# Kernel optimization log

Hardware: AMD Instinct MI355X
Metric: run time of the kernel (lower is better)

The kernel has to match this reference:

```python
import jax, jax.numpy as jnp
import numpy as np

N = 16383        # complete binary tree, 14 levels
D_NODE = 512
D_SSM = 512
D_STATE = 16
MAX_DEPTH = 14   # number of BFS levels (depth 0..13)
LN_EPS = 1e-5


def setup_inputs() -> dict:
    key = jax.random.key(0)
    ks = jax.random.split(key, 8)
    # tree structure: parent[i] = (i-1)//2, root has parent -1; BFS order == index order
    parent = np.concatenate([np.array([-1]), (np.arange(1, N) - 1) // 2]).astype(np.int64)
    depth = np.floor(np.log2(np.arange(N) + 1)).astype(np.int32)
    s = jax.random.normal(ks[0], (N, D_NODE), jnp.float32)
    w = jax.random.uniform(ks[1], (N,), jnp.float32, minval=0.01, maxval=1.0)
    # parameters (xavier-ish scales)
    W_in = jax.random.normal(ks[2], (D_SSM, D_NODE + 1), jnp.float32) * (1.0 / np.sqrt(D_NODE + 1))
    b_in = jnp.zeros((D_SSM,), jnp.float32)
    W_delta = jax.random.normal(ks[3], (D_SSM, D_SSM), jnp.float32) * (1.0 / np.sqrt(D_SSM))
    # dt-style bias init: softplus(b) ~ dt in [1e-3, 1e-1]
    dt = jnp.exp(jax.random.uniform(ks[4], (D_SSM,), jnp.float32) * (np.log(0.1) - np.log(0.001)) + np.log(0.001))
    b_delta = dt + jnp.log(-jnp.expm1(-dt))
    W_w = jax.random.normal(ks[5], (D_SSM, 1), jnp.float32)
    b_w = jnp.zeros((D_SSM,), jnp.float32)
    A_log = jnp.log(jnp.broadcast_to(jnp.arange(1.0, D_STATE + 1.0, dtype=jnp.float32)[None, :], (D_SSM, D_STATE)))
    D = jnp.ones((D_SSM,), jnp.float32)
    W_B = jax.random.normal(ks[6], (D_STATE, D_SSM), jnp.float32) * (1.0 / np.sqrt(D_SSM))
    b_B = jnp.zeros((D_STATE,), jnp.float32)
    W_C = jax.random.normal(ks[7], (D_STATE, D_SSM), jnp.float32) * (1.0 / np.sqrt(D_SSM))
    b_C = jnp.zeros((D_STATE,), jnp.float32)
    gamma = jnp.ones((D_SSM,), jnp.float32)
    beta = jnp.zeros((D_SSM,), jnp.float32)
    return {"s": s, "w": w, "parent": jnp.asarray(parent), "depth": jnp.asarray(depth),
            "W_in": W_in, "b_in": b_in, "W_delta": W_delta, "b_delta": b_delta,
            "W_w": W_w, "b_w": b_w, "A_log": A_log, "D": D,
            "W_B": W_B, "b_B": b_B, "W_C": W_C, "b_C": b_C,
            "gamma": gamma, "beta": beta}


def reference(s, w, parent, depth, W_in, b_in, W_delta, b_delta, W_w, b_w,
              A_log, D, W_B, b_B, W_C, b_C, gamma, beta):
    n = s.shape[0]
    log_w = jnp.log(w + 1e-6)[:, None]                       # [N, 1]
    feat = jnp.concatenate([s, log_w], axis=1)               # [N, d_node+1]
    x = feat @ W_in.T + b_in                                 # [N, d_ssm]
    delta = jax.nn.softplus(x @ W_delta.T + b_delta) * jax.nn.sigmoid(log_w @ W_w.T + b_w)  # [N, d_ssm]
    A = -jnp.exp(A_log)                                      # [d_ssm, d_state]
    B = x @ W_B.T + b_B                                      # [N, d_state]
    C = x @ W_C.T + b_C                                      # [N, d_state]
    A_bar = jnp.exp(delta[:, :, None] * A[None])             # [N, d_ssm, d_state]
    Bx = (delta * x)[:, :, None] * B[:, None, :]             # [N, d_ssm, d_state]
    # level-parallel tree scan: all nodes at BFS depth l updated together
    par = jnp.maximum(parent, 0)
    has_par = (parent >= 0)[:, None, None]
    H = jnp.zeros((n, A_bar.shape[1], A_bar.shape[2]), x.dtype)
    for lvl in range(MAX_DEPTH):
        h_par = jnp.where(has_par, jnp.take(H, par, axis=0), 0.0)
        H = jnp.where((depth == lvl)[:, None, None], A_bar * h_par + Bx, H)
    Y = jnp.einsum('nds,ns->nd', H, C) + D * x               # [N, d_ssm]
    mu = jnp.mean(Y, axis=-1, keepdims=True)
    var = jnp.var(Y, axis=-1, keepdims=True)
    return (Y - mu) / jnp.sqrt(var + LN_EPS) * gamma + beta
```

## Files before the change

kernel.cpp:

```cpp
#include <hip/hip_runtime.h>
#include <hip/hip_bf16.h>
#include <math.h>

#define D_SSM 512
#define D_STATE 16
#define CKPT_BASE 511
#define N_CKPT 512
#define MPAD 16384

typedef __attribute__((ext_vector_type(8))) short short8;
typedef __attribute__((ext_vector_type(4))) float floatx4;

__device__ __forceinline__ unsigned short f2bf(float f) {
    unsigned int u = __float_as_uint(f);
    unsigned int r = (u + 0x7fffu + ((u >> 16) & 1u)) >> 16;
    return (unsigned short)r;
}
__device__ __forceinline__ float bf2f(unsigned short u) {
    return __uint_as_float(((unsigned int)u) << 16);
}
__device__ __forceinline__ void g2lds16(const void* g, void* l) {
    __builtin_amdgcn_global_load_lds(
        (const __attribute__((address_space(1))) void*)g,
        (__attribute__((address_space(3))) void*)l, 16, 0, 0);
}

__device__ __forceinline__ void pw_powers2(float r, float2* p) {
    float r2 = r * r, r4 = r2 * r2, r8 = r4 * r4;
    p[0].x = r;            p[0].y = r2;
    p[1].x = p[0].x * r2;  p[1].y = p[0].y * r2;
    p[2].x = p[0].x * r4;  p[2].y = p[0].y * r4;
    p[3].x = p[1].x * r4;  p[3].y = p[1].y * r4;
    p[4].x = p[0].x * r8;  p[4].y = p[0].y * r8;
    p[5].x = p[1].x * r8;  p[5].y = p[1].y * r8;
    p[6].x = p[2].x * r8;  p[6].y = p[2].y * r8;
    p[7].x = p[3].x * r8;  p[7].y = p[3].y * r8;
}

__global__ __launch_bounds__(256) void prep_kernel(
    const float* __restrict__ s, const float* __restrict__ w,
    const float* __restrict__ W_in, const float* __restrict__ W_delta,
    const float* __restrict__ W_B, const float* __restrict__ W_C,
    const float* __restrict__ A_log,
    unsigned short* __restrict__ s_bf, float* __restrict__ lw,
    unsigned short* __restrict__ Win_bf, unsigned short* __restrict__ Wd_bf,
    float* __restrict__ As_tab, int* __restrict__ fast_tab,
    int Nn)
{
    const int b = blockIdx.x, t = threadIdx.x;
    if (b < 2048) {
        #pragma unroll
        for (int rr = 0; rr < 8; rr++) {
            int row = b * 8 + rr;
            unsigned int pack = 0;
            if (row < Nn) {
                float2 sv = *(const float2*)(s + (size_t)row * 512 + t * 2);
                pack = (unsigned int)f2bf(sv.x) | ((unsigned int)f2bf(sv.y) << 16);
            }
            *(unsigned int*)(s_bf + (size_t)row * 512 + t * 2) = pack;
            if (t == 0) lw[row] = (row < Nn) ? logf(w[row] + 1e-6f) : 0.f;
        }
    } else if (b < 2048 + 512) {
        int c = b - 2048;
        float a0 = W_in[(size_t)c * 513 + t * 2];
        float a1 = W_in[(size_t)c * 513 + t * 2 + 1];
        *(unsigned int*)(Win_bf + (size_t)c * 512 + t * 2) =
            (unsigned int)f2bf(a0) | ((unsigned int)f2bf(a1) << 16);
    } else if (b < 2048 + 1024) {
        int c = b - 2048 - 512;
        float2 wv = *(const float2*)(W_delta + (size_t)c * 512 + t * 2);
        *(unsigned int*)(Wd_bf + (size_t)c * 512 + t * 2) =
            (unsigned int)f2bf(wv.x) | ((unsigned int)f2bf(wv.y) << 16);
    } else if (b < 2048 + 1024 + 128) {
        int c = b - 2048 - 1024;
        float2 wv; wv.x = 0.f; wv.y = 0.f;
        if (c < 16)      wv = *(const float2*)(W_B + (size_t)c * 512 + t * 2);
        else if (c < 32) wv = *(const float2*)(W_C + (size_t)(c - 16) * 512 + t * 2);
        *(unsigned int*)(Wd_bf + (size_t)(512 + c) * 512 + t * 2) =
            (unsigned int)f2bf(wv.x) | ((unsigned int)f2bf(wv.y) << 16);
    } else {
        int ch = (b - (2048 + 1024 + 128)) * 256 + t;
        float As0 = -__expf(A_log[ch * 16]);
        bool ok = true;
        #pragma unroll
        for (int q = 1; q < 16; q++) {
            float As = -__expf(A_log[ch * 16 + q]);
            ok = ok && (fabsf(As - (float)(q + 1) * As0) <= 1e-4f * (float)(q + 1));
        }
        As_tab[ch] = As0;
        fast_tab[ch] = ok ? 1 : 0;
    }
}

__global__ __launch_bounds__(256) void gemm_mfma(
    const unsigned short* __restrict__ Abf,
    const unsigned short* __restrict__ Wbf,
    float* __restrict__ outf,
    unsigned short* __restrict__ outbf,
    const float* __restrict__ bias,
    const float* __restrict__ lw,
    const float* __restrict__ wcol, int wcol_stride,
    const float* __restrict__ bw,
    const float* __restrict__ b_B, const float* __restrict__ b_C,
    float* __restrict__ Bm, float* __restrict__ Cm,
    int mode)
{
    __shared__ __align__(16) short As[2][128 * 32];
    __shared__ __align__(16) short Bs[2][128 * 32];
    const int tid = threadIdx.x;
    const int wave = tid >> 6, lane = tid & 63;

    const int nwg  = gridDim.x * gridDim.y;
    const int orig = blockIdx.y * gridDim.x + blockIdx.x;
    const int wsw  = (orig & 7) * (nwg >> 3) + (orig >> 3);
    const int bx   = wsw % gridDim.x;
    const int by   = wsw / gridDim.x;
    const int row0 = by * 128;
    const int col0 = bx * 128;

    const int wr = (wave >> 1) * 64;
    const int wc = (wave & 1) * 64;

    floatx4 acc[4][4] = {};

    const int srow = lane >> 2;
    const int sg   = (lane & 3) ^ ((srow >> 1) & 3);
    const int scol = sg * 8;

    const unsigned short* Ag = Abf + (size_t)(row0 + wave * 16 + srow) * 512 + scol;
    const unsigned short* Wg = Wbf + (size_t)(col0 + wave * 16 + srow) * 512 + scol;
    char* Al = (char*)&As[0][0] + wave * 1024;
    char* Bl = (char*)&Bs[0][0] + wave * 1024;

    #define STAGE(buf, k0)                                              \
        do {                                                            \
            g2lds16(Ag + (k0),            Al + (buf) * 8192);           \
            g2lds16(Ag + 64 * 512 + (k0), Al + (buf) * 8192 + 4096);    \
            g2lds16(Wg + (k0),            Bl + (buf) * 8192);           \
            g2lds16(Wg + 64 * 512 + (k0), Bl + (buf) * 8192 + 4096);    \
        } while (0)

    STAGE(0, 0);
    __syncthreads();

    for (int it = 0; it < 16; ++it) {
        const int cur = it & 1;
        if (it < 15) STAGE(cur ^ 1, (it + 1) * 32);

        short8 af[4], bfr[4];
        #pragma unroll
        for (int i = 0; i < 4; i++) {
            int m = wr + i * 16 + (lane & 15);
            int gm = (lane >> 4) ^ ((m >> 1) & 3);
            af[i] = *(const short8*)&As[cur][m * 32 + gm * 8];
        }
        #pragma unroll
        for (int j = 0; j < 4; j++) {
            int n = wc + j * 16 + (lane & 15);
            int gn = (lane >> 4) ^ ((n >> 1) & 3);
            bfr[j] = *(const short8*)&Bs[cur][n * 32 + gn * 8];
        }
        #pragma unroll
        for (int i = 0; i < 4; i++)
            #pragma unroll
            for (int j = 0; j < 4; j++)
                acc[i][j] = __builtin_amdgcn_mfma_f32_16x16x32_bf16(af[i], bfr[j], acc[i][j], 0, 0, 0);
        __syncthreads();
    }
    #undef STAGE

    if (col0 >= 512) {
        #pragma unroll
        for (int i = 0; i < 4; i++) {
            #pragma unroll
            for (int reg = 0; reg < 4; reg++) {
                int r = row0 + wr + i * 16 + (lane >> 4) * 4 + reg;
                #pragma unroll
                for (int j = 0; j < 4; j++) {
                    int c2 = wc + j * 16 + (lane & 15);
                    float z = acc[i][j][reg];
                    if (c2 < 16)      Bm[(size_t)r * 16 + c2]        = z + b_B[c2];
                    else if (c2 < 32) Cm[(size_t)r * 16 + (c2 - 16)] = z + b_C[c2 - 16];
                }
            }
        }
        return;
    }

    #pragma unroll
    for (int i = 0; i < 4; i++) {
        #pragma unroll
        for (int reg = 0; reg < 4; reg++) {
            int r = row0 + wr + i * 16 + (lane >> 4) * 4 + reg;
            float lwr = lw[r];
            #pragma unroll
            for (int j = 0; j < 4; j++) {
                int c = col0 + wc + j * 16 + (lane & 15);
                float z = acc[i][j][reg] + bias[c];
                if (mode == 0) {
                    float o = z + lwr * wcol[(size_t)c * wcol_stride];
                    outbf[(size_t)r * 512 + c] = f2bf(o);
                } else {
                    float sp = (z > 15.f) ? z : __logf(1.f + __expf(z));
                    float sg2 = __builtin_amdgcn_rcpf(1.f + __expf(-(lwr * wcol[c] + bw[c])));
                    outf[(size_t)r * 512 + c] = sp * sg2;
                }
            }
        }
    }
}

__global__ __launch_bounds__(512) void scan_fused(
    const unsigned short* __restrict__ x_bf, const float* __restrict__ delta,
    const float* __restrict__ Bm, const float* __restrict__ Cm,
    const float* __restrict__ A_log, const float* __restrict__ Dv,
    const float* __restrict__ gamma, const float* __restrict__ beta,
    const float* __restrict__ As_tab, const int* __restrict__ fast_tab,
    float* __restrict__ out)
{
    __shared__ float Yb[16 * 512];
    __shared__ int nid[16];
    __shared__ float red[16];
    const int bid = blockIdx.x;
    const int d = threadIdx.x;

    const float As0 = As_tab[d];
    const bool fast = fast_tab[d] != 0;
    const float dvd = Dv[d];

    if (bid < 2 * N_CKPT) {
        const int p  = bid & 511;
        const int c0 = bid >> 9;
        const int a9 = CKPT_BASE + p;

        float2 H9[8];
        #pragma unroll
        for (int q = 0; q < 8; q++) { H9[q].x = 0.f; H9[q].y = 0.f; }
        {
            float cum = 0.f;
            int a = a9;
            #pragma unroll
            for (int k = 0; k < 10; k++) {
                float da = delta[(size_t)a * 512 + d];
                float bx = da * bf2f(x_bf[(size_t)a * 512 + d]);
                const float2* B2 = (const float2*)(Bm + (size_t)a * 16);
                if (fast) {
                    float r = __expf(As0 * cum);
                    float2 pw2[8]; pw_powers2(r, pw2);
                    #pragma unroll
                    for (int q = 0; q < 8; q++) {
                        float2 bb = B2[q];
                        H9[q].x = fmaf(bx * pw2[q].x, bb.x, H9[q].x);
                        H9[q].y = fmaf(bx * pw2[q].y, bb.y, H9[q].y);
                    }
                } else {
                    const float* Bn = Bm + (size_t)a * 16;
                    #pragma unroll
                    for (int ss = 0; ss < 16; ss++) {
                        float As = -__expf(A_log[d * 16 + ss]);
                        float h = bx * __expf(As * cum) * Bn[ss];
                        if (ss & 1) H9[ss >> 1].y += h; else H9[ss >> 1].x += h;
                    }
                }
                cum += da;
                a = (a - 1) >> 1;
            }
        }

        auto stepf = [&](int n, const float2* Hp, float2* Hc, int slot) {
            float dlt = delta[(size_t)n * 512 + d];
            float xv = bf2f(x_bf[(size_t)n * 512 + d]);
            float bx = dlt * xv;
            const float2* B2 = (const float2*)(Bm + (size_t)n * 16);
            const float2* C2 = (const float2*)(Cm + (size_t)n * 16);
            float y0 = 0.f, y1 = 0.f;
            if (fast) {
                float r = __expf(As0 * dlt);
                float2 pw2[8]; pw_powers2(r, pw2);
                #pragma unroll
                for (int q = 0; q < 8; q++) {
                    float2 bb = B2[q], cc = C2[q];
                    float2 h;
                    h.x = fmaf(pw2[q].x, Hp[q].x, bx * bb.x);
                    h.y = fmaf(pw2[q].y, Hp[q].y, bx * bb.y);
                    Hc[q] = h;
                    y0 = fmaf(cc.x, h.x, y0);
                    y1 = fmaf(cc.y, h.y, y1);
                }
            } else {
                const float* Bn = Bm + (size_t)n * 16;
                const float* Cn = Cm + (size_t)n * 16;
                #pragma unroll
                for (int ss = 0; ss < 16; ss++) {
                    float Ab = __expf(dlt * (-__expf(A_log[d * 16 + ss])));
                    float hp = (ss & 1) ? Hp[ss >> 1].y : Hp[ss >> 1].x;
                    float h = fmaf(Ab, hp, bx * Bn[ss]);
                    if (ss & 1) Hc[ss >> 1].y = h; else Hc[ss >> 1].x = h;
                    y0 = fmaf(Cn[ss], h, y0);
                }
            }
            Yb[slot * 512 + d] = fmaf(dvd, xv, y0 + y1);
            if (d == 0) nid[slot] = n;
        };
        auto leaff = [&](int n, const float2* Hp, int slot) {
            float dlt = delta[(size_t)n * 512 + d];
            float xv = bf2f(x_bf[(size_t)n * 512 + d]);
            float bx = dlt * xv;
            const float2* B2 = (const float2*)(Bm + (size_t)n * 16);
            const float2* C2 = (const float2*)(Cm + (size_t)n * 16);
            float y0 = 0.f, y1 = 0.f;
            if (fast) {
                float r = __expf(As0 * dlt);
                float2 pw2[8]; pw_powers2(r, pw2);
                #pragma unroll
                for (int q = 0; q < 8; q++) {
                    float2 bb = B2[q], cc = C2[q];
                    float hx = fmaf(pw2[q].x, Hp[q].x, bx * bb.x);
                    float hy = fmaf(pw2[q].y, Hp[q].y, bx * bb.y);
                    y0 = fmaf(cc.x, hx, y0);
                    y1 = fmaf(cc.y, hy, y1);
                }
            } else {
                const float* Bn = Bm + (size_t)n * 16;
                const float* Cn = Cm + (size_t)n * 16;
                #pragma unroll
                for (int ss = 0; ss < 16; ss++) {
                    float Ab = __expf(dlt * (-__expf(A_log[d * 16 + ss])));
                    float hp = (ss & 1) ? Hp[ss >> 1].y : Hp[ss >> 1].x;
                    float h = fmaf(Ab, hp, bx * Bn[ss]);
                    y0 = fmaf(Cn[ss], h, y0);
                }
            }
            Yb[slot * 512 + d] = fmaf(dvd, xv, y0 + y1);
            if (d == 0) nid[slot] = n;
        };

        int slot = 0;
        if (c0 == 0) {
            float xv = bf2f(x_bf[(size_t)a9 * 512 + d]);
            const float2* C2 = (const float2*)(Cm + (size_t)a9 * 16);
            float y0 = 0.f, y1 = 0.f;
            #pragma unroll
            for (int q = 0; q < 8; q++) {
                float2 cc = C2[q];
                y0 = fmaf(cc.x, H9[q].x, y0);
                y1 = fmaf(cc.y, H9[q].y, y1);
            }
            Yb[d] = fmaf(dvd, xv, y0 + y1);
            if (d == 0) nid[0] = a9;
            slot = 1;
        }

        float2 H10[8], H11[8], H12[8];
        const int n10 = 2 * a9 + 1 + c0;
        stepf(n10, H9, H10, slot++);
        #pragma unroll
        for (int c1 = 0; c1 < 2; c1++) {
            int n11 = 2 * n10 + 1 + c1;
            stepf(n11, H10, H11, slot++);
            #pragma unroll
            for (int c2 = 0; c2 < 2; c2++) {
                int n12 = 2 * n11 + 1 + c2;
                stepf(n12, H11, H12, slot++);
                #pragma unroll
                for (int c3 = 0; c3 < 2; c3++) {
                    int n13 = 2 * n12 + 1 + c3;
                    leaff(n13, H12, slot++);
                }
            }
        }
        __syncthreads();

        const int cnt = (c0 == 0) ? 16 : 15;
        const int w = d >> 6, lane = d & 63;
        for (int i = w; i < cnt; i += 8) {
            int n = nid[i];
            float v[8]; float s1 = 0.f, s2 = 0.f;
            #pragma unroll
            for (int k = 0; k < 8; k++) {
                v[k] = Yb[i * 512 + lane + 64 * k];
                s1 += v[k]; s2 += v[k] * v[k];
            }
            #pragma unroll
            for (int off = 32; off > 0; off >>= 1) {
                s1 += __shfl_xor(s1, off);
                s2 += __shfl_xor(s2, off);
            }
            float mu = s1 * (1.f / 512.f);
            float inv = rsqrtf(s2 * (1.f / 512.f) - mu * mu + 1e-5f);
            #pragma unroll
            for (int k = 0; k < 8; k++) {
                int ch = lane + 64 * k;
                out[(size_t)n * 512 + ch] = (v[k] - mu) * inv * gamma[ch] + beta[ch];
            }
        }
    } else {
        const int n = bid - 2 * N_CKPT;

        float2 acc2[8];
        #pragma unroll
        for (int q = 0; q < 8; q++) { acc2[q].x = 0.f; acc2[q].y = 0.f; }

        float cum = 0.f;
        int a = n;
        #pragma unroll
        for (int k = 0; k < 9; k++) {
            if (a >= 0) {
                float da = delta[(size_t)a * 512 + d];
                float bx = da * bf2f(x_bf[(size_t)a * 512 + d]);
                const float2* B2 = (const float2*)(Bm + (size_t)a * 16);
                if (fast) {
                    float r = __expf(As0 * cum);
                    float2 pw2[8]; pw_powers2(r, pw2);
                    #pragma unroll
                    for (int q = 0; q < 8; q++) {
                        float2 bb = B2[q];
                        acc2[q].x = fmaf(bx * pw2[q].x, bb.x, acc2[q].x);
                        acc2[q].y = fmaf(bx * pw2[q].y, bb.y, acc2[q].y);
                    }
                } else {
                    const float* Bn = Bm + (size_t)a * 16;
                    #pragma unroll
                    for (int ss = 0; ss < 16; ss++) {
                        float As = -__expf(A_log[d * 16 + ss]);
                        float h = bx * __expf(As * cum) * Bn[ss];
                        if (ss & 1) acc2[ss >> 1].y += h; else acc2[ss >> 1].x += h;
                    }
                }
                cum += da;
                a = (a - 1) >> 1;
            }
        }

        float xv = bf2f(x_bf[(size_t)n * 512 + d]);
        const float2* C2 = (const float2*)(Cm + (size_t)n * 16);
        float y0 = 0.f, y1 = 0.f;
        #pragma unroll
        for (int q = 0; q < 8; q++) {
            float2 cc = C2[q];
            y0 = fmaf(cc.x, acc2[q].x, y0);
            y1 = fmaf(cc.y, acc2[q].y, y1);
        }
        float y = fmaf(dvd, xv, y0 + y1);

        float s1 = y, s2 = y * y;
        #pragma unroll
        for (int off = 32; off > 0; off >>= 1) {
            s1 += __shfl_xor(s1, off);
            s2 += __shfl_xor(s2, off);
        }
        int wid = d >> 6, lane = d & 63;
        if (lane == 0) { red[wid] = s1; red[wid + 8] = s2; }
        __syncthreads();
        float S1 = 0.f, S2 = 0.f;
        #pragma unroll
        for (int k = 0; k < 8; k++) { S1 += red[k]; S2 += red[k + 8]; }
        float mu = S1 * (1.f / 512.f);
        float var = S2 * (1.f / 512.f) - mu * mu;
        float inv = rsqrtf(var + 1e-5f);
        out[(size_t)n * 512 + d] = (y - mu) * inv * gamma[d] + beta[d];
    }
}

extern "C" void kernel_launch(void* const* d_in, const int* in_sizes, int n_in,
                              void* d_out, int out_size, void* d_ws, size_t ws_size,
                              hipStream_t stream) {
    const float* s_in   = (const float*)d_in[0];
    const float* w      = (const float*)d_in[1];
    const float* W_in    = (const float*)d_in[4];
    const float* b_in    = (const float*)d_in[5];
    const float* W_delta = (const float*)d_in[6];
    const float* b_delta = (const float*)d_in[7];
    const float* W_w     = (const float*)d_in[8];
    const float* b_w     = (const float*)d_in[9];
    const float* A_log   = (const float*)d_in[10];
    const float* Dv      = (const float*)d_in[11];
    const float* W_B     = (const float*)d_in[12];
    const float* b_B     = (const float*)d_in[13];
    const float* W_C     = (const float*)d_in[14];
    const float* b_C     = (const float*)d_in[15];
    const float* gamma   = (const float*)d_in[16];
    const float* beta    = (const float*)d_in[17];
    float* out = (float*)d_out;

    const int Nn = in_sizes[1];

    float* ws    = (float*)d_ws;
    float* lw    = ws;
    float* delta = lw + MPAD;
    float* Bm    = delta + (size_t)MPAD * 512;
    float* Cm    = Bm + (size_t)MPAD * 16;
    unsigned short* s_bf  = (unsigned short*)(Cm + (size_t)MPAD * 16);
    unsigned short* x_bf  = s_bf + (size_t)MPAD * 512;
    unsigned short* Win_bf = x_bf + (size_t)MPAD * 512;
    unsigned short* Wd_bf  = Win_bf + 512 * 512;
    float* As_tab  = (float*)(Wd_bf + 640 * 512);
    int*   fast_tab = (int*)(As_tab + 512);

    prep_kernel<<<2048 + 1024 + 128 + 2, 256, 0, stream>>>(
        s_in, w, W_in, W_delta, W_B, W_C, A_log,
        s_bf, lw, Win_bf, Wd_bf, As_tab, fast_tab, Nn);

    dim3 g1(4, 128);
    gemm_mfma<<<g1, 256, 0, stream>>>(s_bf, Win_bf, nullptr, x_bf,
                                      b_in, lw, W_in + 512, 513, nullptr,
                                      nullptr, nullptr, nullptr, nullptr, 0);
    dim3 g2(5, 128);
    gemm_mfma<<<g2, 256, 0, stream>>>(x_bf, Wd_bf, delta, nullptr,
                                      b_delta, lw, W_w, 1, b_w,
                                      b_B, b_C, Bm, Cm, 1);

    scan_fused<<<2 * N_CKPT + CKPT_BASE, 512, 0, stream>>>(
        x_bf, delta, Bm, Cm, A_log, Dv, gamma, beta, As_tab, fast_tab, out);
}
```

Baseline: 225.0 us.

## Prefetch subtree delta/x rows into LDS and normalize each node inline

Checkpoint blocks now issue async global-to-LDS loads for the delta and x rows of all 15 subtree nodes before the ancestor accumulation, so those loads overlap with the level-9 prefix computation. The step/leaf functions read delta and x from LDS instead of global memory. LayerNorm is now done per node right after its output is computed, using a wave-shuffle plus double-buffered block reduction, replacing the 16x512 Y staging buffer and the separate normalize pass. This adds a __syncthreads per node (about 16 barriers) in exchange for less LDS, fewer uncoalesced global reads, and coalesced per-thread output stores.

New measurement: 239.1 us. 1.06x slower.

```diff
diff --git a/kernel.cpp b/kernel.cpp
--- a/kernel.cpp
+++ b/kernel.cpp
@@ -218,11 +218,13 @@
     const float* __restrict__ As_tab, const int* __restrict__ fast_tab,
     float* __restrict__ out)
 {
-    __shared__ float Yb[16 * 512];
-    __shared__ int nid[16];
-    __shared__ float red[16];
+    __shared__ __align__(16) char SMEMRAW[15 * 512 * 4 + 15 * 512 * 2 + 32 * 4];
+    float* const DL  = (float*)SMEMRAW;
+    unsigned short* const XL = (unsigned short*)(SMEMRAW + 30720);
+    float* const red = (float*)(SMEMRAW + 46080);
     const int bid = blockIdx.x;
     const int d = threadIdx.x;
+    const int wid = d >> 6, lane = d & 63;
 
     const float As0 = As_tab[d];
     const bool fast = fast_tab[d] != 0;
@@ -232,17 +234,38 @@
         const int p  = bid & 511;
         const int c0 = bid >> 9;
         const int a9 = CKPT_BASE + p;
+        const int n10 = 2 * a9 + 1 + c0;
+        const float gm = gamma[d], bt = beta[d];
+
+        for (int i = wid; i < 30; i += 8) {
+            int row = i >> 1, half = i & 1;
+            int v = row + 1;
+            int j = 31 - __builtin_clz((unsigned)v);
+            int node = ((n10 + 1) << j) - 1 + (v - (1 << j));
+            g2lds16(delta + (size_t)node * 512 + half * 256 + lane * 4,
+                    (char*)DL + row * 2048 + half * 1024);
+        }
+        for (int i = wid; i < 15; i += 8) {
+            int v = i + 1;
+            int j = 31 - __builtin_clz((unsigned)v);
+            int node = ((n10 + 1) << j) - 1 + (v - (1 << j));
+            g2lds16(x_bf + (size_t)node * 512 + lane * 8,
+                    (char*)XL + i * 1024);
+        }
 
         float2 H9[8];
         #pragma unroll
         for (int q = 0; q < 8; q++) { H9[q].x = 0.f; H9[q].y = 0.f; }
+        float xv0 = 0.f;
         {
             float cum = 0.f;
             int a = a9;
             #pragma unroll
             for (int k = 0; k < 10; k++) {
                 float da = delta[(size_t)a * 512 + d];
-                float bx = da * bf2f(x_bf[(size_t)a * 512 + d]);
+                float xv = bf2f(x_bf[(size_t)a * 512 + d]);
+                if (k == 0) xv0 = xv;
+                float bx = da * xv;
                 const float2* B2 = (const float2*)(Bm + (size_t)a * 16);
                 if (fast) {
                     float r = __expf(As0 * cum);
@@ -266,10 +289,42 @@
                 a = (a - 1) >> 1;
             }
         }
-
-        auto stepf = [&](int n, const float2* Hp, float2* Hc, int slot) {
-            float dlt = delta[(size_t)n * 512 + d];
-            float xv = bf2f(x_bf[(size_t)n * 512 + d]);
+        __syncthreads();
+
+        int lncnt = 0;
+        auto lnstore = [&](int n, float y) {
+            float s1 = y, s2 = y * y;
+            #pragma unroll
+            for (int off = 32; off > 0; off >>= 1) {
+                s1 += __shfl_xor(s1, off);
+                s2 += __shfl_xor(s2, off);
+            }
+            int bank = (lncnt++ & 1) * 16;
+            if (lane == 0) { red[bank + wid] = s1; red[bank + 8 + wid] = s2; }
+            __syncthreads();
+            float S1 = 0.f, S2 = 0.f;
+            #pragma unroll
+            for (int k = 0; k < 8; k++) { S1 += red[bank + k]; S2 += red[bank + 8 + k]; }
+            float mu = S1 * (1.f / 512.f);
+            float inv = rsqrtf(S2 * (1.f / 512.f) - mu * mu + 1e-5f);
+            out[(size_t)n * 512 + d] = (y - mu) * inv * gm + bt;
+        };
+
+        if (c0 == 0) {
+            const float2* C2 = (const float2*)(Cm + (size_t)a9 * 16);
+            float y0 = 0.f, y1 = 0.f;
+            #pragma unroll
+            for (int q = 0; q < 8; q++) {
+                float2 cc = C2[q];
+                y0 = fmaf(cc.x, H9[q].x, y0);
+                y1 = fmaf(cc.y, H9[q].y, y1);
+            }
+            lnstore(a9, fmaf(dvd, xv0, y0 + y1));
+        }
+
+        auto stepf = [&](int n, int row, const float2* Hp, float2* Hc) {
+            float dlt = DL[row * 512 + d];
+            float xv = bf2f(XL[row * 512 + d]);
             float bx = dlt * xv;
             const float2* B2 = (const float2*)(Bm + (size_t)n * 16);
             const float2* C2 = (const float2*)(Cm + (size_t)n * 16);
@@ -299,99 +354,24 @@
                     y0 = fmaf(Cn[ss], h, y0);
                 }
             }
-            Yb[slot * 512 + d] = fmaf(dvd, xv, y0 + y1);
-            if (d == 0) nid[slot] = n;
+            lnstore(n, fmaf(dvd, xv, y0 + y1));
         };
-        auto leaff = [&](int n, const float2* Hp, int slot) {
-            float dlt = delta[(size_t)n * 512 + d];
-            float xv = bf2f(x_bf[(size_t)n * 512 + d]);
-            float bx = dlt * xv;
-            const float2* B2 = (const float2*)(Bm + (size_t)n * 16);
-            const float2* C2 = (const float2*)(Cm + (size_t)n * 16);
-            float y0 = 0.f, y1 = 0.f;
-            if (fast) {
-                float r = __expf(As0 * dlt);
-                float2 pw2[8]; pw_powers2(r, pw2);
-                #pragma unroll
-                for (int q = 0; q < 8; q++) {
-                    float2 bb = B2[q], cc = C2[q];
-                    float hx = fmaf(pw2[q].x, Hp[q].x, bx * bb.x);
-                    float hy = fmaf(pw2[q].y, Hp[q].y, bx * bb.y);
-                    y0 = fmaf(cc.x, hx, y0);
-                    y1 = fmaf(cc.y, hy, y1);
-                }
-            } else {
-                const float* Bn = Bm + (size_t)n * 16;
-                const float* Cn = Cm + (size_t)n * 16;
-                #pragma unroll
-                for (int ss = 0; ss < 16; ss++) {
-                    float Ab = __expf(dlt * (-__expf(A_log[d * 16 + ss])));
-                    float hp = (ss & 1) ? Hp[ss >> 1].y : Hp[ss >> 1].x;
-                    float h = fmaf(Ab, hp, bx * Bn[ss]);
-                    y0 = fmaf(Cn[ss], h, y0);
-                }
-            }
-            Yb[slot * 512 + d] = fmaf(dvd, xv, y0 + y1);
-            if (d == 0) nid[slot] = n;
-        };
-
-        int slot = 0;
-        if (c0 == 0) {
-            float xv = bf2f(x_bf[(size_t)a9 * 512 + d]);
-            const float2* C2 = (const float2*)(Cm + (size_t)a9 * 16);
-            float y0 = 0.f, y1 = 0.f;
-            #pragma unroll
-            for (int q = 0; q < 8; q++) {
-                float2 cc = C2[q];
-                y0 = fmaf(cc.x, H9[q].x, y0);
-                y1 = fmaf(cc.y, H9[q].y, y1);
-            }
-            Yb[d] = fmaf(dvd, xv, y0 + y1);
-            if (d == 0) nid[0] = a9;
-            slot = 1;
-        }
-
-        float2 H10[8], H11[8], H12[8];
-        const int n10 = 2 * a9 + 1 + c0;
-        stepf(n10, H9, H10, slot++);
+
+        float2 H10[8], H11[8], H12[8], H13[8];
+        stepf(n10, 0, H9, H10);
         #pragma unroll
         for (int c1 = 0; c1 < 2; c1++) {
             int n11 = 2 * n10 + 1 + c1;
-            stepf(n11, H10, H11, slot++);
+            stepf(n11, 1 + c1, H10, H11);
             #pragma unroll
             for (int c2 = 0; c2 < 2; c2++) {
                 int n12 = 2 * n11 + 1 + c2;
-                stepf(n12, H11, H12, slot++);
+                stepf(n12, 3 + 2 * c1 + c2, H11, H12);
                 #pragma unroll
                 for (int c3 = 0; c3 < 2; c3++) {
                     int n13 = 2 * n12 + 1 + c3;
-                    leaff(n13, H12, slot++);
-                }
-            }
-        }
-        __syncthreads();
-
-        const int cnt = (c0 == 0) ? 16 : 15;
-        const int w = d >> 6, lane = d & 63;
-        for (int i = w; i < cnt; i += 8) {
-            int n = nid[i];
-            float v[8]; float s1 = 0.f, s2 = 0.f;
-            #pragma unroll
-            for (int k = 0; k < 8; k++) {
-                v[k] = Yb[i * 512 + lane + 64 * k];
-                s1 += v[k]; s2 += v[k] * v[k];
-            }
-            #pragma unroll
-            for (int off = 32; off > 0; off >>= 1) {
-                s1 += __shfl_xor(s1, off);
-                s2 += __shfl_xor(s2, off);
-            }
-            float mu = s1 * (1.f / 512.f);
-            float inv = rsqrtf(s2 * (1.f / 512.f) - mu * mu + 1e-5f);
-            #pragma unroll
-            for (int k = 0; k < 8; k++) {
-                int ch = lane + 64 * k;
-                out[(size_t)n * 512 + ch] = (v[k] - mu) * inv * gamma[ch] + beta[ch];
+                    stepf(n13, 7 + 4 * c1 + 2 * c2 + c3, H12, H13);
+                }
             }
         }
     } else {
@@ -449,7 +429,6 @@
             s1 += __shfl_xor(s1, off);
             s2 += __shfl_xor(s2, off);
         }
-        int wid = d >> 6, lane = d & 63;
         if (lane == 0) { red[wid] = s1; red[wid + 8] = s2; }
         __syncthreads();
         float S1 = 0.f, S2 = 0.f;
```
